# Performance work log

Measured on AMD Instinct MI355X. Metric: run time of the kernel, lower is better.

The kernel has to match this reference:

```python
import jax, jax.numpy as jnp
import numpy as np

EPS = 1e-12  # torch F.normalize eps

def rmsnorm(x, g, dim):
    # F.normalize(x, dim=-1) * sqrt(dim) * g  (g is a learned scalar)
    n = jnp.maximum(jnp.linalg.norm(x, axis=-1, keepdims=True), EPS)
    return x / n * (dim ** 0.5) * g

def modulate(x, scale, shift):
    # x: (B,T,D); scale/shift: (B,D)
    return x * (1.0 + scale[:, None, :]) + shift[:, None, :]

def setup_inputs() -> dict:
    key = jax.random.key(0)
    ks = jax.random.split(key, 12)
    B, T, D, H = 8, 1024, 1024, 16
    Dm = 4 * D
    s = 0.02
    inp = {
        'x': jax.random.normal(ks[0], (B, T, D), jnp.float32),
        'c': jax.random.normal(ks[1], (B, D), jnp.float32),
        'g1': jnp.ones((1,), jnp.float32),
        'g2': jnp.ones((1,), jnp.float32),
        'gq': jnp.ones((1,), jnp.float32),
        'gk': jnp.ones((1,), jnp.float32),
        'Wqkv': jax.random.normal(ks[2], (3 * D, D), jnp.float32) * s,
        'bqkv': jnp.zeros((3 * D,), jnp.float32),
        'Wproj': jax.random.normal(ks[3], (D, D), jnp.float32) * s,
        'bproj': jnp.zeros((D,), jnp.float32),
        'Wfc1': jax.random.normal(ks[4], (Dm, D), jnp.float32) * s,
        'bfc1': jnp.zeros((Dm,), jnp.float32),
        'Wfc2': jax.random.normal(ks[5], (D, Dm), jnp.float32) * s,
        'bfc2': jnp.zeros((D,), jnp.float32),
        'Wada': jax.random.normal(ks[6], (6 * D, D), jnp.float32) * s,
        'bada': jnp.zeros((6 * D,), jnp.float32),
    }
    return inp

def reference(x, c, g1, g2, gq, gk, Wqkv, bqkv, Wproj, bproj,
              Wfc1, bfc1, Wfc2, bfc2, Wada, bada):
    B, T, D = x.shape
    H = 16
    hd = D // H

    # adaLN modulation: SiLU -> Linear -> chunk 6 along last dim
    ada = jax.nn.silu(c) @ Wada.T + bada  # (B, 6D)
    shift_msa, scale_msa, gate_msa, shift_mlp, scale_mlp, gate_mlp = jnp.split(ada, 6, axis=-1)

    # --- attention branch ---
    h = modulate(rmsnorm(x, g1, D), scale_msa, shift_msa)  # (B,T,D)
    qkv = h @ Wqkv.T + bqkv  # (B,T,3D)
    qkv = qkv.reshape(B, T, 3, H, hd).transpose(2, 0, 3, 1, 4)  # (3,B,H,T,hd)
    q, k, v = qkv[0], qkv[1], qkv[2]
    q = rmsnorm(q, gq, hd) * (hd ** -0.5)
    k = rmsnorm(k, gk, hd)
    attn = jax.nn.softmax(jnp.einsum('bhqd,bhkd->bhqk', q, k), axis=-1)
    o = jnp.einsum('bhqk,bhkd->bhqd', attn, v)  # (B,H,T,hd)
    o = o.transpose(0, 2, 1, 3).reshape(B, T, D)
    o = o @ Wproj.T + bproj
    x = x + gate_msa[:, None, :] * o

    # --- MLP branch ---
    h = modulate(rmsnorm(x, g2, D), scale_mlp, shift_mlp)
    h = jax.nn.gelu(h @ Wfc1.T + bfc1, approximate=True)
    h = h @ Wfc2.T + bfc2
    x = x + gate_mlp[:, None, :] * h
    return x
```

## Files before the change

kernel.cpp:

```cpp
#include <hip/hip_runtime.h>
#include <hip/hip_bf16.h>
#include <math.h>

typedef __bf16 bf16x8 __attribute__((ext_vector_type(8)));
typedef __bf16 bf16x4 __attribute__((ext_vector_type(4)));
typedef float  f32x4  __attribute__((ext_vector_type(4)));

#define DEV static __device__ __forceinline__

DEV unsigned short f2bf(float f) {
    unsigned u = __builtin_bit_cast(unsigned, f);
    u += 0x7fffu + ((u >> 16) & 1u);
    return (unsigned short)(u >> 16);
}
DEV float bf2f(unsigned short u) {
    unsigned x = ((unsigned)u) << 16;
    return __builtin_bit_cast(float, x);
}

__global__ void k_cvt(const float* __restrict__ in, unsigned short* __restrict__ out) {
    int i = (blockIdx.x * 256 + threadIdx.x) * 4;
    float4 v = *(const float4*)(in + i);
    ushort4 o;
    o.x = f2bf(v.x); o.y = f2bf(v.y); o.z = f2bf(v.z); o.w = f2bf(v.w);
    *(ushort4*)(out + i) = o;
}

__global__ void k_ada(const float* __restrict__ c, const float* __restrict__ Wada,
                      const float* __restrict__ bada, float* __restrict__ ada) {
    __shared__ float sc[1024];
    int b = blockIdx.x;
    int tid = threadIdx.x;
    for (int k = tid; k < 1024; k += 256) {
        float x = c[b * 1024 + k];
        sc[k] = x / (1.f + __expf(-x));
    }
    __syncthreads();
    int wid = tid >> 6, lane = tid & 63;
    int n = blockIdx.y * 4 + wid;
    const float* wr = Wada + (size_t)n * 1024;
    float acc = 0.f;
    #pragma unroll
    for (int k = 0; k < 1024; k += 64) acc += sc[k + lane] * wr[k + lane];
    #pragma unroll
    for (int o = 32; o; o >>= 1) acc += __shfl_xor(acc, o);
    if (lane == 0) ada[b * 6144 + n] = acc + bada[n];
}

__global__ void k_norm_mod(const float* __restrict__ x, const float* __restrict__ ada,
                           const float* __restrict__ g, unsigned short* __restrict__ h,
                           int shift_off, int scale_off) {
    int row = blockIdx.x;
    int b = row >> 10;
    int tid = threadIdx.x;
    float4 v = *(const float4*)(x + (size_t)row * 1024 + tid * 4);
    float ss = v.x * v.x + v.y * v.y + v.z * v.z + v.w * v.w;
    #pragma unroll
    for (int o = 32; o; o >>= 1) ss += __shfl_xor(ss, o);
    __shared__ float red[4];
    int wid = tid >> 6, lane = tid & 63;
    if (lane == 0) red[wid] = ss;
    __syncthreads();
    float nrm = sqrtf(red[0] + red[1] + red[2] + red[3]);
    float f = g[0] * 32.f / fmaxf(nrm, 1e-12f);
    float4 s4 = *(const float4*)(ada + b * 6144 + scale_off + tid * 4);
    float4 h4 = *(const float4*)(ada + b * 6144 + shift_off + tid * 4);
    ushort4 o;
    o.x = f2bf(v.x * f * (1.f + s4.x) + h4.x);
    o.y = f2bf(v.y * f * (1.f + s4.y) + h4.y);
    o.z = f2bf(v.z * f * (1.f + s4.z) + h4.z);
    o.w = f2bf(v.w * f * (1.f + s4.w) + h4.w);
    *(ushort4*)(h + (size_t)row * 1024 + tid * 4) = o;
}

template <int EPI>
__global__ __launch_bounds__(256, 4)
void k_gemm4(const unsigned short* __restrict__ A, const unsigned short* __restrict__ Bw,
             const float* __restrict__ bias, int N, int K, int gridM,
             float* __restrict__ outF, unsigned short* __restrict__ outH,
             const float* __restrict__ resid, const float* __restrict__ ada, int gate_off) {
    __shared__ unsigned short lA[128 * 32];
    __shared__ unsigned short lB[128 * 32];
    int tid = threadIdx.x;
    int wid = tid >> 6, lane = tid & 63;
    int li = lane & 15, lg = lane >> 4;
    int bid = blockIdx.x;
    int mb = bid % gridM, nb = bid / gridM;
    int m0 = mb * 128, n0 = nb * 128;
    int wr = (wid >> 1) * 64, wc = (wid & 1) * 64;

    int trow = tid >> 2, tg = tid & 3;
    int tf = (trow & 3) ^ ((trow >> 2) & 3);
    int tgs = (tg ^ tf) * 8;
    int lf = (li & 3) ^ ((li >> 2) & 3);
    int rs = (lg ^ lf) * 8;

    f32x4 acc[4][4] = {};

    for (int kk = 0; kk < K; kk += 32) {
        #pragma unroll
        for (int l = 0; l < 2; ++l) {
            int row = l * 64 + trow;
            const unsigned short* ga = A  + (size_t)(m0 + row) * K + kk + tgs;
            const unsigned short* gb = Bw + (size_t)(n0 + row) * K + kk + tgs;
            unsigned short* la = lA + l * 2048 + wid * 512;
            unsigned short* lb = lB + l * 2048 + wid * 512;
            __builtin_amdgcn_global_load_lds((const __attribute__((address_space(1))) void*)ga,
                                             (__attribute__((address_space(3))) void*)la, 16, 0, 0);
            __builtin_amdgcn_global_load_lds((const __attribute__((address_space(1))) void*)gb,
                                             (__attribute__((address_space(3))) void*)lb, 16, 0, 0);
        }
        __syncthreads();
        bf16x8 af[4];
        #pragma unroll
        for (int i = 0; i < 4; ++i)
            af[i] = *(const bf16x8*)(lA + (wr + i * 16 + li) * 32 + rs);
        #pragma unroll
        for (int j = 0; j < 4; ++j) {
            bf16x8 bfr = *(const bf16x8*)(lB + (wc + j * 16 + li) * 32 + rs);
            #pragma unroll
            for (int i = 0; i < 4; ++i)
                acc[i][j] = __builtin_amdgcn_mfma_f32_16x16x32_bf16(af[i], bfr, acc[i][j], 0, 0, 0);
        }
        __syncthreads();
    }

    int rb4 = lg * 4;
    #pragma unroll
    for (int i = 0; i < 4; ++i) {
        #pragma unroll
        for (int j = 0; j < 4; ++j) {
            #pragma unroll
            for (int r = 0; r < 4; ++r) {
                int row = m0 + wr + i * 16 + rb4 + r;
                int col = n0 + wc + j * 16 + li;
                float vv = acc[i][j][r] + bias[col];
                if (EPI == 0) {
                    outH[(size_t)row * N + col] = f2bf(vv);
                } else if (EPI == 2) {
                    float a2 = 0.7978845608f * (vv + 0.044715f * vv * vv * vv);
                    float e = __expf(-2.f * fabsf(a2));
                    float th = copysignf((1.f - e) / (1.f + e), a2);
                    outH[(size_t)row * N + col] = f2bf(0.5f * vv * (1.f + th));
                } else {
                    int b = row >> 10;
                    float gt = ada[b * 6144 + gate_off + col];
                    outF[(size_t)row * N + col] = resid[(size_t)row * N + col] + gt * vv;
                }
            }
        }
    }
}

__global__ __launch_bounds__(256)
void k_qkv_post(const unsigned short* __restrict__ qkv,
                const float* __restrict__ gq, const float* __restrict__ gk,
                unsigned short* __restrict__ Qb, unsigned short* __restrict__ Kb,
                unsigned short* __restrict__ Vtg) {
    __shared__ unsigned short vt[64 * 72];
    int bh = blockIdx.x;
    int b = bh >> 4, h = bh & 15;
    int t0 = blockIdx.y * 64;
    int tid = threadIdx.x;
    int row = tid >> 2, part = tid & 3;
    size_t rbase = ((size_t)(b * 1024 + t0 + row)) * 3072 + h * 64 + part * 16;
    size_t obase = (size_t)bh * 65536 + (size_t)(t0 + row) * 64 + part * 16;

    #pragma unroll
    for (int s = 0; s < 2; ++s) {
        uint4 u0 = *(const uint4*)(qkv + rbase + s * 1024);
        uint4 u1 = *(const uint4*)(qkv + rbase + s * 1024 + 8);
        float vals[16];
        const unsigned* pu = (const unsigned*)&u0;
        #pragma unroll
        for (int j = 0; j < 4; ++j) {
            vals[2*j]   = bf2f((unsigned short)(pu[j] & 0xffff));
            vals[2*j+1] = bf2f((unsigned short)(pu[j] >> 16));
        }
        pu = (const unsigned*)&u1;
        #pragma unroll
        for (int j = 0; j < 4; ++j) {
            vals[8+2*j]   = bf2f((unsigned short)(pu[j] & 0xffff));
            vals[8+2*j+1] = bf2f((unsigned short)(pu[j] >> 16));
        }
        float ss = 0.f;
        #pragma unroll
        for (int j = 0; j < 16; ++j) ss += vals[j] * vals[j];
        ss += __shfl_xor(ss, 1);
        ss += __shfl_xor(ss, 2);
        float nrm = fmaxf(sqrtf(ss), 1e-12f);
        float fsc = (s == 0 ? gq[0] : 8.f * gk[0]) / nrm;
        uint4 w0, w1;
        unsigned* pw = (unsigned*)&w0;
        #pragma unroll
        for (int j = 0; j < 4; ++j)
            pw[j] = (unsigned)f2bf(vals[2*j] * fsc) | ((unsigned)f2bf(vals[2*j+1] * fsc) << 16);
        pw = (unsigned*)&w1;
        #pragma unroll
        for (int j = 0; j < 4; ++j)
            pw[j] = (unsigned)f2bf(vals[8+2*j] * fsc) | ((unsigned)f2bf(vals[8+2*j+1] * fsc) << 16);
        unsigned short* dst = (s == 0 ? Qb : Kb);
        *(uint4*)(dst + obase)     = w0;
        *(uint4*)(dst + obase + 8) = w1;
    }
    {
        uint4 u0 = *(const uint4*)(qkv + rbase + 2048);
        uint4 u1 = *(const uint4*)(qkv + rbase + 2048 + 8);
        const unsigned* pu = (const unsigned*)&u0;
        #pragma unroll
        for (int j = 0; j < 4; ++j) {
            vt[(part * 16 + 2*j)     * 72 + row] = (unsigned short)(pu[j] & 0xffff);
            vt[(part * 16 + 2*j + 1) * 72 + row] = (unsigned short)(pu[j] >> 16);
        }
        pu = (const unsigned*)&u1;
        #pragma unroll
        for (int j = 0; j < 4; ++j) {
            vt[(part * 16 + 8 + 2*j)     * 72 + row] = (unsigned short)(pu[j] & 0xffff);
            vt[(part * 16 + 8 + 2*j + 1) * 72 + row] = (unsigned short)(pu[j] >> 16);
        }
    }
    __syncthreads();
    {
        int d = tid >> 2, seg = tid & 3;
        uint4 w0 = *(const uint4*)(vt + d * 72 + seg * 16);
        uint4 w1 = *(const uint4*)(vt + d * 72 + seg * 16 + 8);
        size_t vdst = (size_t)bh * 65536 + (size_t)d * 1024 + t0 + seg * 16;
        *(uint4*)(Vtg + vdst)     = w0;
        *(uint4*)(Vtg + vdst + 8) = w1;
    }
}

__global__ __launch_bounds__(256)
void k_attn_mfma(const unsigned short* __restrict__ Qb,
                 const unsigned short* __restrict__ Kb,
                 const unsigned short* __restrict__ Vtg,
                 unsigned short* __restrict__ outp) {
    __shared__ unsigned short Kt[128 * 64];
    __shared__ unsigned short Vl[64 * 136];
    int bh = blockIdx.x;
    int t0 = blockIdx.y * 64;
    int tid = threadIdx.x, wid = tid >> 6, lane = tid & 63;
    int li = lane & 15, lg = lane >> 4;
    const size_t bh64k = (size_t)bh * 65536;

    bf16x8 q0, q1;
    {
        const unsigned short* Qg = Qb + bh64k + (size_t)(t0 + wid * 16 + li) * 64 + lg * 8;
        q0 = *(const bf16x8*)Qg;
        q1 = *(const bf16x8*)(Qg + 32);
    }
    f32x4 oacc[4] = {};
    float den = 0.f;

    for (int kt = 0; kt < 8; ++kt) {
        __syncthreads();
        #pragma unroll
        for (int i = 0; i < 4; ++i) {
            int s = i * 256 + tid;
            int r = s >> 3, c16 = s & 7;
            const unsigned short* src = Kb + bh64k + (size_t)(kt * 128 + r) * 64 + ((c16 ^ (r & 7)) * 8);
            unsigned short* dst = Kt + i * 2048 + wid * 512;
            __builtin_amdgcn_global_load_lds((const __attribute__((address_space(1))) void*)src,
                                             (__attribute__((address_space(3))) void*)dst, 16, 0, 0);
        }
        #pragma unroll
        for (int i = 0; i < 4; ++i) {
            int s = i * 256 + tid;
            int d = s >> 4, k16 = s & 15;
            uint4 v = *(const uint4*)(Vtg + bh64k + (size_t)d * 1024 + kt * 128 + k16 * 8);
            *(uint4*)(Vl + d * 136 + k16 * 8) = v;
        }
        __syncthreads();

        f32x4 st[8];
        #pragma unroll
        for (int f = 0; f < 8; ++f) {
            int row = f * 16 + li;
            bf16x8 a0 = *(const bf16x8*)(Kt + row * 64 + ((lg       ^ (row & 7)) * 8));
            bf16x8 a1 = *(const bf16x8*)(Kt + row * 64 + (((4 + lg) ^ (row & 7)) * 8));
            f32x4 s = {};
            s = __builtin_amdgcn_mfma_f32_16x16x32_bf16(a0, q0, s, 0, 0, 0);
            s = __builtin_amdgcn_mfma_f32_16x16x32_bf16(a1, q1, s, 0, 0, 0);
            f32x4 e;
            e[0] = __expf(s[0]); e[1] = __expf(s[1]);
            e[2] = __expf(s[2]); e[3] = __expf(s[3]);
            den += e[0] + e[1] + e[2] + e[3];
            st[f] = e;
        }
        #pragma unroll
        for (int ks = 0; ks < 4; ++ks) {
            f32x4 e0 = st[2 * ks], e1 = st[2 * ks + 1];
            bf16x8 pa;
            pa[0] = (__bf16)e0[0]; pa[1] = (__bf16)e0[1]; pa[2] = (__bf16)e0[2]; pa[3] = (__bf16)e0[3];
            pa[4] = (__bf16)e1[0]; pa[5] = (__bf16)e1[1]; pa[6] = (__bf16)e1[2]; pa[7] = (__bf16)e1[3];
            #pragma unroll
            for (int df = 0; df < 4; ++df) {
                const unsigned short* vp = Vl + (df * 16 + li) * 136 + ks * 32 + lg * 4;
                bf16x4 v0 = *(const bf16x4*)vp;
                bf16x4 v1 = *(const bf16x4*)(vp + 16);
                bf16x8 vb = __builtin_shufflevector(v0, v1, 0, 1, 2, 3, 4, 5, 6, 7);
                oacc[df] = __builtin_amdgcn_mfma_f32_16x16x32_bf16(pa, vb, oacc[df], 0, 0, 0);
            }
        }
    }
    den += __shfl_xor(den, 16);
    den += __shfl_xor(den, 32);

    int b = bh >> 4, h = bh & 15;
    #pragma unroll
    for (int r2 = 0; r2 < 4; ++r2) {
        float dm = __shfl(den, lg * 4 + r2);
        float inv = 1.f / dm;
        int t = t0 + wid * 16 + lg * 4 + r2;
        #pragma unroll
        for (int df = 0; df < 4; ++df) {
            int col = h * 64 + df * 16 + li;
            outp[((size_t)(b * 1024 + t)) * 1024 + col] = f2bf(oacc[df][r2] * inv);
        }
    }
}

extern "C" void kernel_launch(void* const* d_in, const int* in_sizes, int n_in,
                              void* d_out, int out_size, void* d_ws, size_t ws_size,
                              hipStream_t stream) {
    const float* x     = (const float*)d_in[0];
    const float* c     = (const float*)d_in[1];
    const float* g1    = (const float*)d_in[2];
    const float* g2    = (const float*)d_in[3];
    const float* gq    = (const float*)d_in[4];
    const float* gk    = (const float*)d_in[5];
    const float* Wqkv  = (const float*)d_in[6];
    const float* bqkv  = (const float*)d_in[7];
    const float* Wproj = (const float*)d_in[8];
    const float* bproj = (const float*)d_in[9];
    const float* Wfc1  = (const float*)d_in[10];
    const float* bfc1  = (const float*)d_in[11];
    const float* Wfc2  = (const float*)d_in[12];
    const float* bfc2  = (const float*)d_in[13];
    const float* Wada  = (const float*)d_in[14];
    const float* bada  = (const float*)d_in[15];
    float* out = (float*)d_out;

    char* ws = (char*)d_ws;
    unsigned short* wqkv_bf = (unsigned short*)ws; ws += (size_t)3072 * 1024 * 2;
    unsigned short* wproj_bf= (unsigned short*)ws; ws += (size_t)1024 * 1024 * 2;
    unsigned short* wfc1_bf = (unsigned short*)ws; ws += (size_t)4096 * 1024 * 2;
    unsigned short* wfc2_bf = (unsigned short*)ws; ws += (size_t)4096 * 1024 * 2;
    float* ada = (float*)ws;                       ws += (size_t)8 * 6144 * 4;
    unsigned short* hbuf = (unsigned short*)ws;    ws += (size_t)8192 * 1024 * 2;
    unsigned short* qkvb16 = (unsigned short*)ws;  ws += (size_t)8192 * 3072 * 2;
    unsigned short* Qb  = (unsigned short*)ws;     ws += (size_t)8192 * 64 * 16 * 2;
    unsigned short* Kb  = (unsigned short*)ws;     ws += (size_t)8192 * 64 * 16 * 2;
    unsigned short* Vtg = (unsigned short*)ws;     ws += (size_t)8192 * 64 * 16 * 2;
    unsigned short* fc1out = qkvb16;

    k_cvt<<<3072 * 1024 / 1024, 256, 0, stream>>>(Wqkv,  wqkv_bf);
    k_cvt<<<1024 * 1024 / 1024, 256, 0, stream>>>(Wproj, wproj_bf);
    k_cvt<<<4096 * 1024 / 1024, 256, 0, stream>>>(Wfc1,  wfc1_bf);
    k_cvt<<<4096 * 1024 / 1024, 256, 0, stream>>>(Wfc2,  wfc2_bf);
    k_ada<<<dim3(8, 1536), 256, 0, stream>>>(c, Wada, bada, ada);
    k_norm_mod<<<8192, 256, 0, stream>>>(x, ada, g1, hbuf, 0, 1024);
    k_gemm4<0><<<1536, 256, 0, stream>>>(hbuf, wqkv_bf, bqkv, 3072, 1024, 64,
                                         nullptr, qkvb16, nullptr, nullptr, 0);
    k_qkv_post<<<dim3(128, 16), 256, 0, stream>>>(qkvb16, gq, gk, Qb, Kb, Vtg);
    k_attn_mfma<<<dim3(128, 16), 256, 0, stream>>>(Qb, Kb, Vtg, hbuf);
    k_gemm4<1><<<512, 256, 0, stream>>>(hbuf, wproj_bf, bproj, 1024, 1024, 64,
                                        out, nullptr, x, ada, 2048);
    k_norm_mod<<<8192, 256, 0, stream>>>(out, ada, g2, hbuf, 3072, 4096);
    k_gemm4<2><<<2048, 256, 0, stream>>>(hbuf, wfc1_bf, bfc1, 4096, 1024, 64,
                                         nullptr, fc1out, nullptr, nullptr, 0);
    k_gemm4<3><<<512, 256, 0, stream>>>(fc1out, wfc2_bf, bfc2, 1024, 4096, 64,
                                        out, nullptr, out, ada, 5120);
}
```

Measured before the change: 430.4 us.

## Use 64-wide K tiles, split-K for N=1024 GEMMs, and fuse residual with norm

The GEMM kernel now loads 64-wide K slices into LDS with an 8-way XOR swizzle, halving the number of barrier-separated iterations. The two N=1024 GEMMs (proj and fc2) use 2-way split-K (1024 blocks instead of 512) to fill the GPU better, writing bf16 partials into the Q/K scratch buffers. A new kernel sums the partials, adds bias, gate and residual, and fuses the second RMSNorm+modulate, replacing the separate norm launch. Storing partials in bf16 adds rounding error and extra memory traffic for the partial buffers.

```diff
diff --git a/kernel.cpp b/kernel.cpp
--- a/kernel.cpp
+++ b/kernel.cpp
@@ -75,57 +75,71 @@
 
 template <int EPI>
 __global__ __launch_bounds__(256, 4)
-void k_gemm4(const unsigned short* __restrict__ A, const unsigned short* __restrict__ Bw,
-             const float* __restrict__ bias, int N, int K, int gridM,
-             float* __restrict__ outF, unsigned short* __restrict__ outH,
-             const float* __restrict__ resid, const float* __restrict__ ada, int gate_off) {
-    __shared__ unsigned short lA[128 * 32];
-    __shared__ unsigned short lB[128 * 32];
+void k_gemm5(const unsigned short* __restrict__ A, const unsigned short* __restrict__ Bw,
+             const float* __restrict__ bias, int N, int K, int gridM, int gridN, int Kc,
+             unsigned short* __restrict__ outH) {
+    __shared__ unsigned short lA[128 * 64];
+    __shared__ unsigned short lB[128 * 64];
     int tid = threadIdx.x;
     int wid = tid >> 6, lane = tid & 63;
     int li = lane & 15, lg = lane >> 4;
     int bid = blockIdx.x;
-    int mb = bid % gridM, nb = bid / gridM;
+    int mb = bid % gridM;
+    int nb = (bid / gridM) % gridN;
+    int sp = bid / (gridM * gridN);
     int m0 = mb * 128, n0 = nb * 128;
+    int k0 = sp * Kc;
     int wr = (wid >> 1) * 64, wc = (wid & 1) * 64;
 
-    int trow = tid >> 2, tg = tid & 3;
-    int tf = (trow & 3) ^ ((trow >> 2) & 3);
-    int tgs = (tg ^ tf) * 8;
-    int lf = (li & 3) ^ ((li >> 2) & 3);
-    int rs = (lg ^ lf) * 8;
+    int trow = tid >> 3;
+    int gcol = ((tid & 7) ^ (trow & 7)) * 8;
+    int sl0 = (lg ^ (li & 7)) * 8;
+    int sl1 = ((4 + lg) ^ (li & 7)) * 8;
 
     f32x4 acc[4][4] = {};
 
-    for (int kk = 0; kk < K; kk += 32) {
-        #pragma unroll
-        for (int l = 0; l < 2; ++l) {
-            int row = l * 64 + trow;
-            const unsigned short* ga = A  + (size_t)(m0 + row) * K + kk + tgs;
-            const unsigned short* gb = Bw + (size_t)(n0 + row) * K + kk + tgs;
-            unsigned short* la = lA + l * 2048 + wid * 512;
-            unsigned short* lb = lB + l * 2048 + wid * 512;
+    for (int kk = 0; kk < Kc; kk += 64) {
+        #pragma unroll
+        for (int l = 0; l < 4; ++l) {
+            int row = l * 32 + trow;
+            const unsigned short* ga = A  + (size_t)(m0 + row) * K + k0 + kk + gcol;
+            const unsigned short* gb = Bw + (size_t)(n0 + row) * K + k0 + kk + gcol;
+            unsigned short* la = lA + (l * 256 + wid * 64) * 8;
+            unsigned short* lb = lB + (l * 256 + wid * 64) * 8;
             __builtin_amdgcn_global_load_lds((const __attribute__((address_space(1))) void*)ga,
                                              (__attribute__((address_space(3))) void*)la, 16, 0, 0);
             __builtin_amdgcn_global_load_lds((const __attribute__((address_space(1))) void*)gb,
                                              (__attribute__((address_space(3))) void*)lb, 16, 0, 0);
         }
         __syncthreads();
-        bf16x8 af[4];
+        bf16x8 af[4], bfr[4];
         #pragma unroll
         for (int i = 0; i < 4; ++i)
-            af[i] = *(const bf16x8*)(lA + (wr + i * 16 + li) * 32 + rs);
-        #pragma unroll
-        for (int j = 0; j < 4; ++j) {
-            bf16x8 bfr = *(const bf16x8*)(lB + (wc + j * 16 + li) * 32 + rs);
+            af[i] = *(const bf16x8*)(lA + (wr + i * 16 + li) * 64 + sl0);
+        #pragma unroll
+        for (int j = 0; j < 4; ++j)
+            bfr[j] = *(const bf16x8*)(lB + (wc + j * 16 + li) * 64 + sl0);
+        #pragma unroll
+        for (int i = 0; i < 4; ++i)
             #pragma unroll
-            for (int i = 0; i < 4; ++i)
-                acc[i][j] = __builtin_amdgcn_mfma_f32_16x16x32_bf16(af[i], bfr, acc[i][j], 0, 0, 0);
-        }
+            for (int j = 0; j < 4; ++j)
+                acc[i][j] = __builtin_amdgcn_mfma_f32_16x16x32_bf16(af[i], bfr[j], acc[i][j], 0, 0, 0);
+        #pragma unroll
+        for (int i = 0; i < 4; ++i)
+            af[i] = *(const bf16x8*)(lA + (wr + i * 16 + li) * 64 + sl1);
+        #pragma unroll
+        for (int j = 0; j < 4; ++j)
+            bfr[j] = *(const bf16x8*)(lB + (wc + j * 16 + li) * 64 + sl1);
+        #pragma unroll
+        for (int i = 0; i < 4; ++i)
+            #pragma unroll
+            for (int j = 0; j < 4; ++j)
+                acc[i][j] = __builtin_amdgcn_mfma_f32_16x16x32_bf16(af[i], bfr[j], acc[i][j], 0, 0, 0);
         __syncthreads();
     }
 
     int rb4 = lg * 4;
+    size_t poff = (size_t)sp * ((size_t)8192 * N);
     #pragma unroll
     for (int i = 0; i < 4; ++i) {
         #pragma unroll
@@ -134,22 +148,75 @@
             for (int r = 0; r < 4; ++r) {
                 int row = m0 + wr + i * 16 + rb4 + r;
                 int col = n0 + wc + j * 16 + li;
-                float vv = acc[i][j][r] + bias[col];
                 if (EPI == 0) {
-                    outH[(size_t)row * N + col] = f2bf(vv);
+                    outH[(size_t)row * N + col] = f2bf(acc[i][j][r] + bias[col]);
                 } else if (EPI == 2) {
+                    float vv = acc[i][j][r] + bias[col];
                     float a2 = 0.7978845608f * (vv + 0.044715f * vv * vv * vv);
                     float e = __expf(-2.f * fabsf(a2));
                     float th = copysignf((1.f - e) / (1.f + e), a2);
                     outH[(size_t)row * N + col] = f2bf(0.5f * vv * (1.f + th));
                 } else {
-                    int b = row >> 10;
-                    float gt = ada[b * 6144 + gate_off + col];
-                    outF[(size_t)row * N + col] = resid[(size_t)row * N + col] + gt * vv;
+                    outH[poff + (size_t)row * N + col] = f2bf(acc[i][j][r]);
                 }
             }
         }
     }
+}
+
+__global__ void k_fix_norm(const float* __restrict__ x, const unsigned short* __restrict__ P,
+                           const float* __restrict__ bias, const float* __restrict__ ada,
+                           const float* __restrict__ g2, float* __restrict__ out,
+                           unsigned short* __restrict__ h2) {
+    int row = blockIdx.x, b = row >> 10, tid = threadIdx.x;
+    int c = tid * 4;
+    size_t base = (size_t)row * 1024 + c;
+    ushort4 p0 = *(const ushort4*)(P + base);
+    ushort4 p1 = *(const ushort4*)(P + 8388608 + base);
+    float4 xv = *(const float4*)(x + base);
+    float4 bi = *(const float4*)(bias + c);
+    float4 gt = *(const float4*)(ada + b * 6144 + 2048 + c);
+    float4 v;
+    v.x = xv.x + gt.x * (bf2f(p0.x) + bf2f(p1.x) + bi.x);
+    v.y = xv.y + gt.y * (bf2f(p0.y) + bf2f(p1.y) + bi.y);
+    v.z = xv.z + gt.z * (bf2f(p0.z) + bf2f(p1.z) + bi.z);
+    v.w = xv.w + gt.w * (bf2f(p0.w) + bf2f(p1.w) + bi.w);
+    *(float4*)(out + base) = v;
+    float ss = v.x * v.x + v.y * v.y + v.z * v.z + v.w * v.w;
+    #pragma unroll
+    for (int o = 32; o; o >>= 1) ss += __shfl_xor(ss, o);
+    __shared__ float red[4];
+    int wid = tid >> 6, lane = tid & 63;
+    if (lane == 0) red[wid] = ss;
+    __syncthreads();
+    float nrm = sqrtf(red[0] + red[1] + red[2] + red[3]);
+    float f = g2[0] * 32.f / fmaxf(nrm, 1e-12f);
+    float4 sc = *(const float4*)(ada + b * 6144 + 4096 + c);
+    float4 sh = *(const float4*)(ada + b * 6144 + 3072 + c);
+    ushort4 o;
+    o.x = f2bf(v.x * f * (1.f + sc.x) + sh.x);
+    o.y = f2bf(v.y * f * (1.f + sc.y) + sh.y);
+    o.z = f2bf(v.z * f * (1.f + sc.z) + sh.z);
+    o.w = f2bf(v.w * f * (1.f + sc.w) + sh.w);
+    *(ushort4*)(h2 + base) = o;
+}
+
+__global__ void k_fixf(const unsigned short* __restrict__ P, const float* __restrict__ bias,
+                       const float* __restrict__ ada, float* __restrict__ out) {
+    int row = blockIdx.x, b = row >> 10, tid = threadIdx.x;
+    int c = tid * 4;
+    size_t base = (size_t)row * 1024 + c;
+    ushort4 p0 = *(const ushort4*)(P + base);
+    ushort4 p1 = *(const ushort4*)(P + 8388608 + base);
+    float4 xv = *(const float4*)(out + base);
+    float4 bi = *(const float4*)(bias + c);
+    float4 gt = *(const float4*)(ada + b * 6144 + 5120 + c);
+    float4 v;
+    v.x = xv.x + gt.x * (bf2f(p0.x) + bf2f(p1.x) + bi.x);
+    v.y = xv.y + gt.y * (bf2f(p0.y) + bf2f(p1.y) + bi.y);
+    v.z = xv.z + gt.z * (bf2f(p0.z) + bf2f(p1.z) + bi.z);
+    v.w = xv.w + gt.w * (bf2f(p0.w) + bf2f(p1.w) + bi.w);
+    *(float4*)(out + base) = v;
 }
 
 __global__ __launch_bounds__(256)
@@ -353,6 +420,8 @@
     unsigned short* Kb  = (unsigned short*)ws;     ws += (size_t)8192 * 64 * 16 * 2;
     unsigned short* Vtg = (unsigned short*)ws;     ws += (size_t)8192 * 64 * 16 * 2;
     unsigned short* fc1out = qkvb16;
+    unsigned short* Pp = Qb;
+    unsigned short* Pf = Kb;
 
     k_cvt<<<3072 * 1024 / 1024, 256, 0, stream>>>(Wqkv,  wqkv_bf);
     k_cvt<<<1024 * 1024 / 1024, 256, 0, stream>>>(Wproj, wproj_bf);
@@ -360,15 +429,12 @@
     k_cvt<<<4096 * 1024 / 1024, 256, 0, stream>>>(Wfc2,  wfc2_bf);
     k_ada<<<dim3(8, 1536), 256, 0, stream>>>(c, Wada, bada, ada);
     k_norm_mod<<<8192, 256, 0, stream>>>(x, ada, g1, hbuf, 0, 1024);
-    k_gemm4<0><<<1536, 256, 0, stream>>>(hbuf, wqkv_bf, bqkv, 3072, 1024, 64,
-                                         nullptr, qkvb16, nullptr, nullptr, 0);
+    k_gemm5<0><<<1536, 256, 0, stream>>>(hbuf, wqkv_bf, bqkv, 3072, 1024, 64, 24, 1024, qkvb16);
     k_qkv_post<<<dim3(128, 16), 256, 0, stream>>>(qkvb16, gq, gk, Qb, Kb, Vtg);
     k_attn_mfma<<<dim3(128, 16), 256, 0, stream>>>(Qb, Kb, Vtg, hbuf);
-    k_gemm4<1><<<512, 256, 0, stream>>>(hbuf, wproj_bf, bproj, 1024, 1024, 64,
-                                        out, nullptr, x, ada, 2048);
-    k_norm_mod<<<8192, 256, 0, stream>>>(out, ada, g2, hbuf, 3072, 4096);
-    k_gemm4<2><<<2048, 256, 0, stream>>>(hbuf, wfc1_bf, bfc1, 4096, 1024, 64,
-                                         nullptr, fc1out, nullptr, nullptr, 0);
-    k_gemm4<3><<<512, 256, 0, stream>>>(fc1out, wfc2_bf, bfc2, 1024, 4096, 64,
-                                        out, nullptr, out, ada, 5120);
-}
+    k_gemm5<4><<<1024, 256, 0, stream>>>(hbuf, wproj_bf, bproj, 1024, 1024, 64, 8, 512, Pp);
+    k_fix_norm<<<8192, 256, 0, stream>>>(x, Pp, bproj, ada, g2, out, hbuf);
+    k_gemm5<2><<<2048, 256, 0, stream>>>(hbuf, wfc1_bf, bfc1, 4096, 1024, 64, 32, 1024, fc1out);
+    k_gemm5<4><<<1024, 256, 0, stream>>>(fc1out, wfc2_bf, bfc2, 1024, 4096, 64, 8, 2048, Pf);
+    k_fixf<<<8192, 256, 0, stream>>>(Pf, bfc2, ada, out);
+}
```

New measurement: 401.6 us. -6.7%, faster.
